# Optimization experiments

Hardware: AMD Instinct MI355X
Metric: run time of the kernel (lower is better)

## Reference

```python
import jax, jax.numpy as jnp
import numpy as np

SQRT2 = 1.4142135623730951
MH_C = 0.8673250705840776  # (2/sqrt(3)) * pi**(-1/4), mexican-hat normalizer


def _bn(x, eps=1e-5):
    # BatchNorm (training-mode batch stats, default affine gamma=1, beta=0)
    mu = jnp.mean(x, axis=0, keepdims=True)
    var = jnp.var(x, axis=0, keepdims=True)
    return (x - mu) / jnp.sqrt(var + eps)


def setup_inputs() -> dict:
    key = jax.random.key(0)
    ks = jax.random.split(key, 10)
    N, F, E, B, OUT = 1024, 1024, 32768, 16, 10
    H = F // 2  # 512 after Haar DWT
    x = jax.random.normal(ks[0], (N, F), dtype=jnp.float32)
    edge_index = jax.random.randint(ks[1], (2, E), 0, N, dtype=jnp.int32)
    batch = jnp.sort(jax.random.randint(ks[2], (N,), 0, B, dtype=jnp.int32))
    w_att = jax.random.normal(ks[3], (2,), dtype=jnp.float32)  # Linear(2,1,bias=False)
    wk_scale = jnp.ones((H, H), dtype=jnp.float32)
    wk_trans = jax.random.normal(ks[4], (H, H), dtype=jnp.float32) * 0.1
    wk_wav_w = jax.random.normal(ks[5], (H, H), dtype=jnp.float32) * 0.05
    wk_base_w = jax.random.normal(ks[6], (H, H), dtype=jnp.float32) * 0.05
    fc1_w = jax.random.normal(ks[7], (512, F + H), dtype=jnp.float32) * 0.02
    fc1_b = jnp.zeros((512,), dtype=jnp.float32)
    fc2_w = jax.random.normal(ks[8], (OUT, 512), dtype=jnp.float32) * 0.02
    fc2_b = jnp.zeros((OUT,), dtype=jnp.float32)
    return {"x": x, "w_att": w_att, "wk_scale": wk_scale, "wk_trans": wk_trans,
            "wk_wav_w": wk_wav_w, "wk_base_w": wk_base_w, "fc1_w": fc1_w,
            "fc1_b": fc1_b, "fc2_w": fc2_w, "fc2_b": fc2_b,
            "edge_index": edge_index, "batch": batch, "num_graphs": B}


def reference(x, w_att, wk_scale, wk_trans, wk_wav_w, wk_base_w,
              fc1_w, fc1_b, fc2_w, fc2_b, edge_index, batch, num_graphs):
    N = x.shape[0]
    # --- WaveletAttention: Haar ('db1') DWT over the feature dim ---
    xe, xo = x[:, 0::2], x[:, 1::2]
    low = (xe + xo) / SQRT2            # [N, 512]
    high = (xe - xo) / SQRT2           # [N, 512]
    scores = jax.nn.sigmoid(low * w_att[0] + high * w_att[1])
    h = scores * low + (1.0 - scores) * high
    # --- GINConv aggregation (eps=0): self + sum of neighbor features ---
    src, dst = edge_index[0], edge_index[1]
    agg = h + jax.ops.segment_sum(h[src], dst, num_segments=N)  # [N, 512]
    # --- WavKAN layer 512->512 (mexican hat) ---
    xs = (agg[:, None, :] - wk_trans) / wk_scale                # [N, 512, 512]
    xs2 = xs * xs
    mh = MH_C * (1.0 - xs2) * jnp.exp(-0.5 * xs2)
    wav = jnp.einsum('noi,oi->no', mh, wk_wav_w)                # [N, 512]
    base = jax.nn.silu(agg) @ wk_base_w.T
    conv_out = _bn(wav + base)   # WavKAN-internal BatchNorm1d
    conv_out = _bn(conv_out)     # bn1 (dropout p=0 -> identity)
    # --- skip concat + bn2 ---
    z = _bn(jnp.concatenate([x, conv_out], axis=1))             # [N, 1536]
    # --- global mean pool over graphs ---
    sums = jax.ops.segment_sum(z, batch, num_segments=num_graphs)
    cnts = jax.ops.segment_sum(jnp.ones((N,), z.dtype), batch, num_segments=num_graphs)
    pooled = sums / jnp.maximum(cnts, 1.0)[:, None]             # [B, 1536]
    # --- classifier head (eval-mode dropout = identity) ---
    h1 = jax.nn.relu(pooled @ fc1_w.T + fc1_b)
    return h1 @ fc2_w.T + fc2_b
```

## Files before the change

### kernel.cpp

```cpp
#include <hip/hip_runtime.h>
#include <math.h>

#define N_NODES 1024
#define F_DIM   1024
#define H_DIM   512
#define E_EDGES 32768
#define B_GRAPHS 16
#define OUT_DIM 10
#define FH_DIM  1536
#define EPS 1e-5f
#define MH_C_D 0.8673250705840776
#define C2_D   0.72134752044448170368
#define CSC    0.84932180028801904272f
#define WC2F   ((float)(MH_C_D / C2_D))
#define INV_SQRT2 0.70710678118654752440f

typedef float v2f __attribute__((ext_vector_type(2)));
typedef unsigned int u32;
typedef const __attribute__((address_space(1))) u32 gu32;
typedef __attribute__((address_space(3))) u32 lu32;

#if __has_builtin(__builtin_amdgcn_exp2f)
#define EXP2NEG(x) __builtin_amdgcn_exp2f(-(x))
#else
#define EXP2NEG(x) __expf(-0.69314718055994530942f * (x))
#endif

__global__ __launch_bounds__(256) void k_h(const float* __restrict__ x,
                                           const float* __restrict__ watt,
                                           float* __restrict__ h) {
    int idx = blockIdx.x * 256 + threadIdx.x;
    float2 p = ((const float2*)x)[idx];
    float lo = (p.x + p.y) * INV_SQRT2;
    float hi = (p.x - p.y) * INV_SQRT2;
    float t  = lo * watt[0] + hi * watt[1];
    float sc = 1.0f / (1.0f + __expf(-t));
    h[idx] = sc * lo + (1.0f - sc) * hi;
}

__global__ __launch_bounds__(256) void k_zero(float* __restrict__ p) {
    p[blockIdx.x * 256 + threadIdx.x] = 0.0f;
}

__global__ __launch_bounds__(256) void k_hist(const int* __restrict__ dst,
                                              int* __restrict__ deg) {
    int e = blockIdx.x * 256 + threadIdx.x;
    atomicAdd(&deg[dst[e]], 1);
}

__global__ __launch_bounds__(1024) void k_scan(const int* __restrict__ deg,
                                               int* __restrict__ start,
                                               int* __restrict__ cursor) {
    __shared__ int wsum[16];
    int t = threadIdx.x;
    int lane = t & 63, wid = t >> 6;
    int v = deg[t];
    int x = v;
    #pragma unroll
    for (int off = 1; off < 64; off <<= 1) {
        int y = __shfl_up(x, off, 64);
        if (lane >= off) x += y;
    }
    if (lane == 63) wsum[wid] = x;
    __syncthreads();
    if (t < 16) {
        int w = wsum[t];
        int xs = w;
        #pragma unroll
        for (int off = 1; off < 16; off <<= 1) {
            int y = __shfl_up(xs, off, 64);
            if (t >= off) xs += y;
        }
        wsum[t] = xs - w;
    }
    __syncthreads();
    int excl = wsum[wid] + x - v;
    start[t] = excl;
    cursor[t] = excl;
}

__global__ __launch_bounds__(256) void k_fill(const int* __restrict__ src,
                                              const int* __restrict__ dst,
                                              int* __restrict__ cursor,
                                              int* __restrict__ elist) {
    int e = blockIdx.x * 256 + threadIdx.x;
    int slot = atomicAdd(&cursor[dst[e]], 1);
    elist[slot] = src[e];
}

__global__ __launch_bounds__(256) void k_gather(const float* __restrict__ h,
                                                const int* __restrict__ start,
                                                const int* __restrict__ deg,
                                                const int* __restrict__ elist,
                                                float* __restrict__ agg) {
    int d = blockIdx.x;
    int t = threadIdx.x;
    int st = start[d], dg = deg[d];
    const float2* h2 = (const float2*)h;
    float2 a = h2[d * 256 + t];
    int k = 0;
    for (; k + 2 <= dg; k += 2) {
        int s0 = elist[st + k];
        int s1 = elist[st + k + 1];
        float2 v0 = h2[s0 * 256 + t];
        float2 v1 = h2[s1 * 256 + t];
        a.x += v0.x + v1.x;
        a.y += v0.y + v1.y;
    }
    if (k < dg) {
        int s0 = elist[st + k];
        float2 v0 = h2[s0 * 256 + t];
        a.x += v0.x; a.y += v0.y;
    }
    ((float2*)agg)[d * 256 + t] = a;
}

__global__ __launch_bounds__(256) void k_transpose(const float* __restrict__ agg,
                                                   float* __restrict__ aggT,
                                                   float* __restrict__ siluT) {
    __shared__ float tile[64 * 65];
    const int t = threadIdx.x;
    const int n0 = blockIdx.x * 64;
    const int i0 = blockIdx.y * 64;
    #pragma unroll
    for (int v = 0; v < 4; ++v) {
        int flat = v * 256 + t;
        int r = flat >> 4, c4 = flat & 15;
        float4 a = *(const float4*)&agg[(n0 + r) * H_DIM + i0 + c4 * 4];
        tile[(c4 * 4 + 0) * 65 + r] = a.x;
        tile[(c4 * 4 + 1) * 65 + r] = a.y;
        tile[(c4 * 4 + 2) * 65 + r] = a.z;
        tile[(c4 * 4 + 3) * 65 + r] = a.w;
    }
    __syncthreads();
    #pragma unroll
    for (int v = 0; v < 4; ++v) {
        int flat = v * 256 + t;
        int il = flat >> 4, c4 = flat & 15;
        float4 a;
        a.x = tile[il * 65 + c4 * 4 + 0];
        a.y = tile[il * 65 + c4 * 4 + 1];
        a.z = tile[il * 65 + c4 * 4 + 2];
        a.w = tile[il * 65 + c4 * 4 + 3];
        int g = (i0 + il) * N_NODES + n0 + c4 * 4;
        *(float4*)&aggT[g] = a;
        float4 s;
        s.x = a.x / (1.0f + __expf(-a.x));
        s.y = a.y / (1.0f + __expf(-a.y));
        s.z = a.z / (1.0f + __expf(-a.z));
        s.w = a.w / (1.0f + __expf(-a.w));
        *(float4*)&siluT[g] = s;
    }
}

__global__ __launch_bounds__(256) void k_prep(const float* __restrict__ scale,
                                              const float* __restrict__ trans,
                                              const float* __restrict__ ww,
                                              const float* __restrict__ bw,
                                              float* __restrict__ pk) {
    int g = blockIdx.x * 256 + threadIdx.x;
    float iv = 1.0f / scale[g];
    float4 p;
    p.x = iv * CSC;
    p.y = trans[g] * iv * CSC;
    p.z = ww[g] * WC2F;
    p.w = bw[g];
    ((float4*)pk)[g] = p;
}

#define TN 64
#define TO 32
#define KI 16
#define TOP (TO + 1)
#define ZSPLIT 8
#define ZLEN (H_DIM / ZSPLIT)
__global__ __launch_bounds__(256, 4) void k_wavelet(const float* __restrict__ aggT,
                                                    const float* __restrict__ siluT,
                                                    const float* __restrict__ pk,
                                                    float* __restrict__ vbp) {
    __shared__ float sA[KI * TN];
    __shared__ float sS[KI * TN];
    __shared__ float4 sP4[KI * TOP];

    const int t  = threadIdx.x;
    const int n0 = blockIdx.x * TN;
    const int o0 = blockIdx.y * TO;
    const int z0 = blockIdx.z * ZLEN;
    const int nl = (t & 15) * 4;
    const int ol = (t >> 4) * 2;

    v2f accw[2][2] = {};
    v2f accb[2][2] = {};
    const v2f c2v = {(float)C2_D, (float)C2_D};

    for (int stg = 0; stg < ZLEN / KI; ++stg) {
        const int i0 = z0 + stg * KI;
        __syncthreads();
        {
            int g = (i0 + (t >> 4)) * N_NODES + n0 + nl;
            __builtin_amdgcn_global_load_lds((gu32*)&aggT[g],  (lu32*)&sA[t * 4], 16, 0, 0);
            __builtin_amdgcn_global_load_lds((gu32*)&siluT[g], (lu32*)&sS[t * 4], 16, 0, 0);
        }
        #pragma unroll
        for (int j = 0; j < 2; ++j) {
            int u = j * 256 + t;
            int o = u >> 4, ii = u & 15;
            sP4[ii * TOP + o] = ((const float4*)pk)[(o0 + o) * H_DIM + i0 + ii];
        }
        __syncthreads();
        #pragma unroll 4
        for (int ii = 0; ii < KI; ++ii) {
            float4 a = *(const float4*)&sA[ii * TN + nl];
            float4 s = *(const float4*)&sS[ii * TN + nl];
            v2f a01 = {a.x, a.y}, a23 = {a.z, a.w};
            v2f s01 = {s.x, s.y}, s23 = {s.z, s.w};
            #pragma unroll
            for (int oo = 0; oo < 2; ++oo) {
                float4 p = sP4[ii * TOP + ol + oo];
                v2f iv2 = {p.x, p.x};
                v2f tf2 = {p.y, p.y};
                v2f w2  = {p.z, p.z};
                v2f b2  = {p.w, p.w};
                {
                    v2f y  = a01 * iv2 - tf2;
                    v2f y2 = y * y;
                    v2f e; e.x = EXP2NEG(y2.x); e.y = EXP2NEG(y2.y);
                    v2f wm = w2 * (c2v - y2);
                    accw[oo][0] += wm * e;
                    accb[oo][0] += s01 * b2;
                }
                {
                    v2f y  = a23 * iv2 - tf2;
                    v2f y2 = y * y;
                    v2f e; e.x = EXP2NEG(y2.x); e.y = EXP2NEG(y2.y);
                    v2f wm = w2 * (c2v - y2);
                    accw[oo][1] += wm * e;
                    accb[oo][1] += s23 * b2;
                }
            }
        }
    }
    float* out = vbp + (size_t)blockIdx.z * (N_NODES * H_DIM);
    #pragma unroll
    for (int nn = 0; nn < 4; ++nn) {
        int pr = nn >> 1, cmu = nn & 1;
        float2 o2;
        o2.x = (cmu ? accw[0][pr].y : accw[0][pr].x) + (cmu ? accb[0][pr].y : accb[0][pr].x);
        o2.y = (cmu ? accw[1][pr].y : accw[1][pr].x) + (cmu ? accb[1][pr].y : accb[1][pr].x);
        *(float2*)&out[(n0 + nl + nn) * H_DIM + o0 + ol] = o2;
    }
}

__global__ __launch_bounds__(256) void k_reduce(const float* __restrict__ vbp,
                                                float* __restrict__ vb,
                                                float* __restrict__ colsum,
                                                float* __restrict__ colsum2) {
    const int b = blockIdx.x;
    const int o0 = (b & 7) * 64;
    const int n0 = (b >> 3) * 128;
    const int t = threadIdx.x;
    const int oc = o0 + (t & 63);
    const int nsub = t >> 6;
    float s = 0.f, s2 = 0.f;
    for (int r = 0; r < 32; ++r) {
        int n = n0 + r * 4 + nsub;
        size_t idx = (size_t)n * H_DIM + oc;
        float v = 0.f;
        #pragma unroll
        for (int z = 0; z < ZSPLIT; ++z) v += vbp[z * (N_NODES * H_DIM) + idx];
        vb[idx] = v;
        s += v; s2 += v * v;
    }
    __shared__ float sh1[256], sh2[256];
    sh1[t] = s; sh2[t] = s2;
    __syncthreads();
    if (t < 64) {
        s  = sh1[t] + sh1[t + 64] + sh1[t + 128] + sh1[t + 192];
        s2 = sh2[t] + sh2[t + 64] + sh2[t + 128] + sh2[t + 192];
        unsafeAtomicAdd(&colsum[o0 + t], s);
        unsafeAtomicAdd(&colsum2[o0 + t], s2);
    }
}

__global__ __launch_bounds__(256) void k_xstats(const float* __restrict__ x,
                                                float* __restrict__ xsum,
                                                float* __restrict__ xsum2) {
    const int n0 = blockIdx.x * 16;
    const int t = threadIdx.x;
    float s[4] = {}, s2[4] = {};
    for (int r = 0; r < 16; ++r) {
        #pragma unroll
        for (int ch = 0; ch < 4; ++ch) {
            float v = x[(n0 + r) * F_DIM + ch * 256 + t];
            s[ch] += v; s2[ch] += v * v;
        }
    }
    #pragma unroll
    for (int ch = 0; ch < 4; ++ch) {
        unsafeAtomicAdd(&xsum[ch * 256 + t], s[ch]);
        unsafeAtomicAdd(&xsum2[ch * 256 + t], s2[ch]);
    }
}

__global__ __launch_bounds__(256) void k_finalize(const float* __restrict__ colsum,
                                                  const float* __restrict__ colsum2,
                                                  const float* __restrict__ xsum,
                                                  const float* __restrict__ xsum2,
                                                  float* __restrict__ muv,
                                                  float* __restrict__ Sv,
                                                  float* __restrict__ mux,
                                                  float* __restrict__ Sx,
                                                  const int* __restrict__ batch,
                                                  int* __restrict__ gstart,
                                                  int* __restrict__ gcnt) {
    __shared__ int cnt_sh[B_GRAPHS];
    __shared__ int start_sh[B_GRAPHS];
    int t = threadIdx.x;
    if (t < B_GRAPHS) { cnt_sh[t] = 0; start_sh[t] = 0; }
    __syncthreads();
    for (int n = t; n < N_NODES; n += 256) {
        int b = batch[n];
        atomicAdd(&cnt_sh[b], 1);
        if (n == 0 || batch[n - 1] != b) start_sh[b] = n;
    }
    for (int c = t; c < FH_DIM; c += 256) {
        if (c < H_DIM) {
            float mu  = colsum[c] * (1.0f / N_NODES);
            float var = colsum2[c] * (1.0f / N_NODES) - mu * mu;
            if (var < 0.f) var = 0.f;
            float s1v = 1.0f / sqrtf(var + EPS);
            float v1  = var * s1v * s1v;
            float s2v = 1.0f / sqrtf(v1 + EPS);
            float v2  = v1 * s2v * s2v;
            float s3v = 1.0f / sqrtf(v2 + EPS);
            muv[c] = mu;
            Sv[c]  = s1v * s2v * s3v;
        } else {
            int xc = c - H_DIM;
            float mu  = xsum[xc] * (1.0f / N_NODES);
            float var = xsum2[xc] * (1.0f / N_NODES) - mu * mu;
            if (var < 0.f) var = 0.f;
            mux[xc] = mu;
            Sx[xc]  = 1.0f / sqrtf(var + EPS);
        }
    }
    __syncthreads();
    if (t < B_GRAPHS) { gstart[t] = start_sh[t]; gcnt[t] = cnt_sh[t]; }
}

__global__ __launch_bounds__(256) void k_pool(const float* __restrict__ x,
                                              const float* __restrict__ vb,
                                              const int* __restrict__ gstart,
                                              const int* __restrict__ gcnt,
                                              const float* __restrict__ mux,
                                              const float* __restrict__ Sx,
                                              const float* __restrict__ muv,
                                              const float* __restrict__ Sv,
                                              float* __restrict__ pooled) {
    const int b = blockIdx.x;
    const int ch = blockIdx.y;
    const int t = threadIdx.x;
    const int cnt = gcnt[b], st = gstart[b];
    float ic = (cnt > 0) ? 1.0f / (float)cnt : 0.f;
    float acc = 0.f;
    if (ch < 4) {
        const float* base = x + ch * 256 + t;
        for (int r = 0; r < cnt; ++r) acc += base[(size_t)(st + r) * F_DIM];
        int c = ch * 256 + t;
        pooled[b * FH_DIM + c] = (acc * ic - mux[c]) * Sx[c];
    } else {
        int chv = ch - 4;
        const float* base = vb + chv * 256 + t;
        for (int r = 0; r < cnt; ++r) acc += base[(size_t)(st + r) * H_DIM];
        int c = chv * 256 + t;
        pooled[b * FH_DIM + F_DIM + c] = (acc * ic - muv[c]) * Sv[c];
    }
}

__global__ __launch_bounds__(256) void k_fc1(const float* __restrict__ pooled,
                                             const float* __restrict__ w,
                                             const float* __restrict__ bias,
                                             float* __restrict__ h1) {
    int wid = (blockIdx.x * 256 + threadIdx.x) >> 6;
    int lane = threadIdx.x & 63;
    int b = wid >> 9, o = wid & 511;
    const float4* pr = (const float4*)(pooled + b * FH_DIM);
    const float4* wr = (const float4*)(w + o * FH_DIM);
    float acc = 0.f;
    #pragma unroll
    for (int k = 0; k < 6; ++k) {
        float4 a = pr[k * 64 + lane];
        float4 v = wr[k * 64 + lane];
        acc += a.x * v.x + a.y * v.y + a.z * v.z + a.w * v.w;
    }
    #pragma unroll
    for (int off = 32; off > 0; off >>= 1) acc += __shfl_down(acc, off);
    if (lane == 0) h1[b * H_DIM + o] = fmaxf(acc + bias[o], 0.f);
}

__global__ __launch_bounds__(256) void k_fc2(const float* __restrict__ h1,
                                             const float* __restrict__ w,
                                             const float* __restrict__ bias,
                                             float* __restrict__ outp) {
    int wid = (blockIdx.x * 256 + threadIdx.x) >> 6;
    int lane = threadIdx.x & 63;
    if (wid >= B_GRAPHS * OUT_DIM) return;
    int b = wid / OUT_DIM, u = wid % OUT_DIM;
    const float4* hr = (const float4*)(h1 + b * H_DIM);
    const float4* wr = (const float4*)(w + u * H_DIM);
    float acc = 0.f;
    #pragma unroll
    for (int k = 0; k < 2; ++k) {
        float4 a = hr[k * 64 + lane];
        float4 v = wr[k * 64 + lane];
        acc += a.x * v.x + a.y * v.y + a.z * v.z + a.w * v.w;
    }
    #pragma unroll
    for (int off = 32; off > 0; off >>= 1) acc += __shfl_down(acc, off);
    if (lane == 0) outp[b * OUT_DIM + u] = acc + bias[u];
}

extern "C" void kernel_launch(void* const* d_in, const int* in_sizes, int n_in,
                              void* d_out, int out_size, void* d_ws, size_t ws_size,
                              hipStream_t stream) {
    const float* x       = (const float*)d_in[0];
    const float* w_att   = (const float*)d_in[1];
    const float* wk_scale= (const float*)d_in[2];
    const float* wk_trans= (const float*)d_in[3];
    const float* wk_wav  = (const float*)d_in[4];
    const float* wk_base = (const float*)d_in[5];
    const float* fc1_w   = (const float*)d_in[6];
    const float* fc1_b   = (const float*)d_in[7];
    const float* fc2_w   = (const float*)d_in[8];
    const float* fc2_b   = (const float*)d_in[9];
    const int*   eidx    = (const int*)d_in[10];
    const int*   batch   = (const int*)d_in[11];
    float* outp = (float*)d_out;

    float* ws = (float*)d_ws;
    const int NH = N_NODES * H_DIM;
    float* h      = ws;
    float* agg    = h + NH;
    float* aggT   = agg + NH;
    float* siluT  = aggT + NH;
    float* pk     = siluT + NH;
    float* vbp    = pk + 4 * (H_DIM * H_DIM);
    float* vb     = vbp + (size_t)ZSPLIT * NH;
    float* colsum = vb + NH;
    float* colsum2= colsum + 512;
    float* xsum   = colsum2 + 512;
    float* xsum2  = xsum + 1024;
    int*   deg    = (int*)(xsum2 + 1024);
    int*   estart = deg + N_NODES;
    int*   cursor = estart + N_NODES;
    int*   elist  = cursor + N_NODES;
    float* muv    = (float*)(elist + E_EDGES);
    float* Sv     = muv + 512;
    float* mux    = Sv + 512;
    float* Sx     = mux + 1024;
    int*   gstart = (int*)(Sx + 1024);
    int*   gcnt   = gstart + 16;
    float* pooled = (float*)(gcnt + 16);
    float* h1     = pooled + B_GRAPHS * FH_DIM;

    const int* src = eidx;
    const int* dst = eidx + E_EDGES;

    k_zero<<<16, 256, 0, stream>>>(colsum);
    k_h<<<NH / 256, 256, 0, stream>>>(x, w_att, h);
    k_hist<<<E_EDGES / 256, 256, 0, stream>>>(dst, deg);
    k_scan<<<1, N_NODES, 0, stream>>>(deg, estart, cursor);
    k_fill<<<E_EDGES / 256, 256, 0, stream>>>(src, dst, cursor, elist);
    k_prep<<<(H_DIM * H_DIM) / 256, 256, 0, stream>>>(wk_scale, wk_trans, wk_wav, wk_base, pk);
    k_xstats<<<64, 256, 0, stream>>>(x, xsum, xsum2);
    k_gather<<<N_NODES, 256, 0, stream>>>(h, estart, deg, elist, agg);
    {
        dim3 grid(N_NODES / 64, H_DIM / 64);
        k_transpose<<<grid, 256, 0, stream>>>(agg, aggT, siluT);
    }
    {
        dim3 grid(N_NODES / TN, H_DIM / TO, ZSPLIT);
        k_wavelet<<<grid, 256, 0, stream>>>(aggT, siluT, pk, vbp);
    }
    k_reduce<<<64, 256, 0, stream>>>(vbp, vb, colsum, colsum2);
    k_finalize<<<1, 256, 0, stream>>>(colsum, colsum2, xsum, xsum2, muv, Sv, mux, Sx,
                                      batch, gstart, gcnt);
    {
        dim3 grid(B_GRAPHS, 6);
        k_pool<<<grid, 256, 0, stream>>>(x, vb, gstart, gcnt, mux, Sx, muv, Sv, pooled);
    }
    k_fc1<<<(B_GRAPHS * H_DIM * 64) / 256, 256, 0, stream>>>(pooled, fc1_w, fc1_b, h1);
    k_fc2<<<(B_GRAPHS * OUT_DIM * 64 + 255) / 256, 256, 0, stream>>>(h1, fc2_w, fc2_b, outp);
}
```

Before: 214.7 us.

## Merge setup kernels, widen wavelet output tile, fold finalize into pooling

Several small kernels are merged into fewer launches: h computation, parameter packing and zeroing go into one setup kernel, and the degree histogram shares a launch with the x statistics. The finalize kernel is removed, and each pool block now recomputes its graph range and BN scales itself. The wavelet kernel tile grows from 32 to 64 outputs per block, doubling register accumulators so parameter loads are reused across more work. The Mexican-hat multiply is refactored to save an op per element, the gather loop is unrolled by four, and the reduce kernel uses more blocks. The aim is less launch overhead and better reuse, at the cost of higher register pressure and lower occupancy in the wavelet kernel.

```diff
diff --git a/kernel.cpp b/kernel.cpp
--- a/kernel.cpp
+++ b/kernel.cpp
@@ -11,6 +11,7 @@
 #define EPS 1e-5f
 #define MH_C_D 0.8673250705840776
 #define C2_D   0.72134752044448170368
+#define C2_F   ((float)C2_D)
 #define CSC    0.84932180028801904272f
 #define WC2F   ((float)(MH_C_D / C2_D))
 #define INV_SQRT2 0.70710678118654752440f
@@ -26,26 +27,65 @@
 #define EXP2NEG(x) __expf(-0.69314718055994530942f * (x))
 #endif
 
-__global__ __launch_bounds__(256) void k_h(const float* __restrict__ x,
-                                           const float* __restrict__ watt,
-                                           float* __restrict__ h) {
-    int idx = blockIdx.x * 256 + threadIdx.x;
-    float2 p = ((const float2*)x)[idx];
-    float lo = (p.x + p.y) * INV_SQRT2;
-    float hi = (p.x - p.y) * INV_SQRT2;
-    float t  = lo * watt[0] + hi * watt[1];
-    float sc = 1.0f / (1.0f + __expf(-t));
-    h[idx] = sc * lo + (1.0f - sc) * hi;
-}
-
-__global__ __launch_bounds__(256) void k_zero(float* __restrict__ p) {
-    p[blockIdx.x * 256 + threadIdx.x] = 0.0f;
-}
-
-__global__ __launch_bounds__(256) void k_hist(const int* __restrict__ dst,
-                                              int* __restrict__ deg) {
-    int e = blockIdx.x * 256 + threadIdx.x;
-    atomicAdd(&deg[dst[e]], 1);
+__global__ __launch_bounds__(256) void k_setup(const float* __restrict__ x,
+                                               const float* __restrict__ watt,
+                                               float* __restrict__ h,
+                                               const float* __restrict__ scale,
+                                               const float* __restrict__ trans,
+                                               const float* __restrict__ ww,
+                                               const float* __restrict__ bw,
+                                               float* __restrict__ pk,
+                                               float* __restrict__ zbase) {
+    const int bid = blockIdx.x;
+    const int t = threadIdx.x;
+    if (bid < 2048) {
+        int idx = bid * 256 + t;
+        float2 p = ((const float2*)x)[idx];
+        float lo = (p.x + p.y) * INV_SQRT2;
+        float hi = (p.x - p.y) * INV_SQRT2;
+        float tt = lo * watt[0] + hi * watt[1];
+        float sc = 1.0f / (1.0f + __expf(-tt));
+        h[idx] = sc * lo + (1.0f - sc) * hi;
+    } else if (bid < 3072) {
+        int g = (bid - 2048) * 256 + t;
+        float iv = 1.0f / scale[g];
+        float4 p;
+        p.x = iv * CSC;
+        p.y = trans[g] * iv * CSC;
+        p.z = ww[g] * WC2F;
+        p.w = bw[g];
+        ((float4*)pk)[g] = p;
+    } else {
+        zbase[(bid - 3072) * 256 + t] = 0.0f;
+    }
+}
+
+__global__ __launch_bounds__(256) void k_hx(const int* __restrict__ dst,
+                                            int* __restrict__ deg,
+                                            const float* __restrict__ x,
+                                            float* __restrict__ xsum,
+                                            float* __restrict__ xsum2) {
+    const int bid = blockIdx.x;
+    const int t = threadIdx.x;
+    if (bid < 128) {
+        int e = bid * 256 + t;
+        atomicAdd(&deg[dst[e]], 1);
+    } else {
+        const int n0 = (bid - 128) * 16;
+        float s[4] = {}, s2[4] = {};
+        for (int r = 0; r < 16; ++r) {
+            #pragma unroll
+            for (int ch = 0; ch < 4; ++ch) {
+                float v = x[(n0 + r) * F_DIM + ch * 256 + t];
+                s[ch] += v; s2[ch] += v * v;
+            }
+        }
+        #pragma unroll
+        for (int ch = 0; ch < 4; ++ch) {
+            unsafeAtomicAdd(&xsum[ch * 256 + t], s[ch]);
+            unsafeAtomicAdd(&xsum2[ch * 256 + t], s2[ch]);
+        }
+    }
 }
 
 __global__ __launch_bounds__(1024) void k_scan(const int* __restrict__ deg,
@@ -99,15 +139,19 @@
     const float2* h2 = (const float2*)h;
     float2 a = h2[d * 256 + t];
     int k = 0;
-    for (; k + 2 <= dg; k += 2) {
+    for (; k + 4 <= dg; k += 4) {
         int s0 = elist[st + k];
         int s1 = elist[st + k + 1];
+        int s2 = elist[st + k + 2];
+        int s3 = elist[st + k + 3];
         float2 v0 = h2[s0 * 256 + t];
         float2 v1 = h2[s1 * 256 + t];
-        a.x += v0.x + v1.x;
-        a.y += v0.y + v1.y;
-    }
-    if (k < dg) {
+        float2 v2 = h2[s2 * 256 + t];
+        float2 v3 = h2[s3 * 256 + t];
+        a.x += (v0.x + v1.x) + (v2.x + v3.x);
+        a.y += (v0.y + v1.y) + (v2.y + v3.y);
+    }
+    for (; k < dg; ++k) {
         int s0 = elist[st + k];
         float2 v0 = h2[s0 * 256 + t];
         a.x += v0.x; a.y += v0.y;
@@ -153,31 +197,16 @@
     }
 }
 
-__global__ __launch_bounds__(256) void k_prep(const float* __restrict__ scale,
-                                              const float* __restrict__ trans,
-                                              const float* __restrict__ ww,
-                                              const float* __restrict__ bw,
-                                              float* __restrict__ pk) {
-    int g = blockIdx.x * 256 + threadIdx.x;
-    float iv = 1.0f / scale[g];
-    float4 p;
-    p.x = iv * CSC;
-    p.y = trans[g] * iv * CSC;
-    p.z = ww[g] * WC2F;
-    p.w = bw[g];
-    ((float4*)pk)[g] = p;
-}
-
 #define TN 64
-#define TO 32
+#define TO 64
 #define KI 16
 #define TOP (TO + 1)
 #define ZSPLIT 8
 #define ZLEN (H_DIM / ZSPLIT)
-__global__ __launch_bounds__(256, 4) void k_wavelet(const float* __restrict__ aggT,
-                                                    const float* __restrict__ siluT,
-                                                    const float* __restrict__ pk,
-                                                    float* __restrict__ vbp) {
+__global__ __launch_bounds__(256) void k_wavelet(const float* __restrict__ aggT,
+                                                 const float* __restrict__ siluT,
+                                                 const float* __restrict__ pk,
+                                                 float* __restrict__ vbp) {
     __shared__ float sA[KI * TN];
     __shared__ float sS[KI * TN];
     __shared__ float4 sP4[KI * TOP];
@@ -187,11 +216,10 @@
     const int o0 = blockIdx.y * TO;
     const int z0 = blockIdx.z * ZLEN;
     const int nl = (t & 15) * 4;
-    const int ol = (t >> 4) * 2;
-
-    v2f accw[2][2] = {};
-    v2f accb[2][2] = {};
-    const v2f c2v = {(float)C2_D, (float)C2_D};
+    const int ol = (t >> 4) * 4;
+
+    v2f accw[4][2] = {};
+    v2f accb[4][2] = {};
 
     for (int stg = 0; stg < ZLEN / KI; ++stg) {
         const int i0 = z0 + stg * KI;
@@ -202,7 +230,7 @@
             __builtin_amdgcn_global_load_lds((gu32*)&siluT[g], (lu32*)&sS[t * 4], 16, 0, 0);
         }
         #pragma unroll
-        for (int j = 0; j < 2; ++j) {
+        for (int j = 0; j < 4; ++j) {
             int u = j * 256 + t;
             int o = u >> 4, ii = u & 15;
             sP4[ii * TOP + o] = ((const float4*)pk)[(o0 + o) * H_DIM + i0 + ii];
@@ -215,17 +243,19 @@
             v2f a01 = {a.x, a.y}, a23 = {a.z, a.w};
             v2f s01 = {s.x, s.y}, s23 = {s.z, s.w};
             #pragma unroll
-            for (int oo = 0; oo < 2; ++oo) {
+            for (int oo = 0; oo < 4; ++oo) {
                 float4 p = sP4[ii * TOP + ol + oo];
+                float wcs = p.z * C2_F;
                 v2f iv2 = {p.x, p.x};
                 v2f tf2 = {p.y, p.y};
                 v2f w2  = {p.z, p.z};
+                v2f wc2 = {wcs, wcs};
                 v2f b2  = {p.w, p.w};
                 {
                     v2f y  = a01 * iv2 - tf2;
                     v2f y2 = y * y;
                     v2f e; e.x = EXP2NEG(y2.x); e.y = EXP2NEG(y2.y);
-                    v2f wm = w2 * (c2v - y2);
+                    v2f wm = wc2 - w2 * y2;
                     accw[oo][0] += wm * e;
                     accb[oo][0] += s01 * b2;
                 }
@@ -233,7 +263,7 @@
                     v2f y  = a23 * iv2 - tf2;
                     v2f y2 = y * y;
                     v2f e; e.x = EXP2NEG(y2.x); e.y = EXP2NEG(y2.y);
-                    v2f wm = w2 * (c2v - y2);
+                    v2f wm = wc2 - w2 * y2;
                     accw[oo][1] += wm * e;
                     accb[oo][1] += s23 * b2;
                 }
@@ -244,10 +274,12 @@
     #pragma unroll
     for (int nn = 0; nn < 4; ++nn) {
         int pr = nn >> 1, cmu = nn & 1;
-        float2 o2;
-        o2.x = (cmu ? accw[0][pr].y : accw[0][pr].x) + (cmu ? accb[0][pr].y : accb[0][pr].x);
-        o2.y = (cmu ? accw[1][pr].y : accw[1][pr].x) + (cmu ? accb[1][pr].y : accb[1][pr].x);
-        *(float2*)&out[(n0 + nl + nn) * H_DIM + o0 + ol] = o2;
+        float4 o4;
+        o4.x = cmu ? accw[0][pr].y + accb[0][pr].y : accw[0][pr].x + accb[0][pr].x;
+        o4.y = cmu ? accw[1][pr].y + accb[1][pr].y : accw[1][pr].x + accb[1][pr].x;
+        o4.z = cmu ? accw[2][pr].y + accb[2][pr].y : accw[2][pr].x + accb[2][pr].x;
+        o4.w = cmu ? accw[3][pr].y + accb[3][pr].y : accw[3][pr].x + accb[3][pr].x;
+        *(float4*)&out[(n0 + nl + nn) * H_DIM + o0 + ol] = o4;
     }
 }
 
@@ -257,12 +289,12 @@
                                                 float* __restrict__ colsum2) {
     const int b = blockIdx.x;
     const int o0 = (b & 7) * 64;
-    const int n0 = (b >> 3) * 128;
+    const int n0 = (b >> 3) * 64;
     const int t = threadIdx.x;
     const int oc = o0 + (t & 63);
     const int nsub = t >> 6;
     float s = 0.f, s2 = 0.f;
-    for (int r = 0; r < 32; ++r) {
+    for (int r = 0; r < 16; ++r) {
         int n = n0 + r * 4 + nsub;
         size_t idx = (size_t)n * H_DIM + oc;
         float v = 0.f;
@@ -282,98 +314,59 @@
     }
 }
 
-__global__ __launch_bounds__(256) void k_xstats(const float* __restrict__ x,
-                                                float* __restrict__ xsum,
-                                                float* __restrict__ xsum2) {
-    const int n0 = blockIdx.x * 16;
-    const int t = threadIdx.x;
-    float s[4] = {}, s2[4] = {};
-    for (int r = 0; r < 16; ++r) {
-        #pragma unroll
-        for (int ch = 0; ch < 4; ++ch) {
-            float v = x[(n0 + r) * F_DIM + ch * 256 + t];
-            s[ch] += v; s2[ch] += v * v;
-        }
-    }
-    #pragma unroll
-    for (int ch = 0; ch < 4; ++ch) {
-        unsafeAtomicAdd(&xsum[ch * 256 + t], s[ch]);
-        unsafeAtomicAdd(&xsum2[ch * 256 + t], s2[ch]);
-    }
-}
-
-__global__ __launch_bounds__(256) void k_finalize(const float* __restrict__ colsum,
-                                                  const float* __restrict__ colsum2,
-                                                  const float* __restrict__ xsum,
-                                                  const float* __restrict__ xsum2,
-                                                  float* __restrict__ muv,
-                                                  float* __restrict__ Sv,
-                                                  float* __restrict__ mux,
-                                                  float* __restrict__ Sx,
-                                                  const int* __restrict__ batch,
-                                                  int* __restrict__ gstart,
-                                                  int* __restrict__ gcnt) {
-    __shared__ int cnt_sh[B_GRAPHS];
-    __shared__ int start_sh[B_GRAPHS];
-    int t = threadIdx.x;
-    if (t < B_GRAPHS) { cnt_sh[t] = 0; start_sh[t] = 0; }
-    __syncthreads();
-    for (int n = t; n < N_NODES; n += 256) {
-        int b = batch[n];
-        atomicAdd(&cnt_sh[b], 1);
-        if (n == 0 || batch[n - 1] != b) start_sh[b] = n;
-    }
-    for (int c = t; c < FH_DIM; c += 256) {
-        if (c < H_DIM) {
-            float mu  = colsum[c] * (1.0f / N_NODES);
-            float var = colsum2[c] * (1.0f / N_NODES) - mu * mu;
-            if (var < 0.f) var = 0.f;
-            float s1v = 1.0f / sqrtf(var + EPS);
-            float v1  = var * s1v * s1v;
-            float s2v = 1.0f / sqrtf(v1 + EPS);
-            float v2  = v1 * s2v * s2v;
-            float s3v = 1.0f / sqrtf(v2 + EPS);
-            muv[c] = mu;
-            Sv[c]  = s1v * s2v * s3v;
-        } else {
-            int xc = c - H_DIM;
-            float mu  = xsum[xc] * (1.0f / N_NODES);
-            float var = xsum2[xc] * (1.0f / N_NODES) - mu * mu;
-            if (var < 0.f) var = 0.f;
-            mux[xc] = mu;
-            Sx[xc]  = 1.0f / sqrtf(var + EPS);
-        }
-    }
-    __syncthreads();
-    if (t < B_GRAPHS) { gstart[t] = start_sh[t]; gcnt[t] = cnt_sh[t]; }
-}
-
 __global__ __launch_bounds__(256) void k_pool(const float* __restrict__ x,
                                               const float* __restrict__ vb,
-                                              const int* __restrict__ gstart,
-                                              const int* __restrict__ gcnt,
-                                              const float* __restrict__ mux,
-                                              const float* __restrict__ Sx,
-                                              const float* __restrict__ muv,
-                                              const float* __restrict__ Sv,
+                                              const int* __restrict__ batch,
+                                              const float* __restrict__ colsum,
+                                              const float* __restrict__ colsum2,
+                                              const float* __restrict__ xsum,
+                                              const float* __restrict__ xsum2,
                                               float* __restrict__ pooled) {
     const int b = blockIdx.x;
     const int ch = blockIdx.y;
     const int t = threadIdx.x;
-    const int cnt = gcnt[b], st = gstart[b];
+
+    __shared__ int s_cnt[4];
+    __shared__ int s_st;
+    int c = 0;
+    for (int n = t; n < N_NODES; n += 256) {
+        int bb = batch[n];
+        int pb = (n == 0) ? -1 : batch[n - 1];
+        c += (bb == b) ? 1 : 0;
+        if (bb == b && pb != b) s_st = n;
+    }
+    #pragma unroll
+    for (int off = 32; off > 0; off >>= 1) c += __shfl_down(c, off);
+    if ((t & 63) == 0) s_cnt[t >> 6] = c;
+    __syncthreads();
+    int cnt = s_cnt[0] + s_cnt[1] + s_cnt[2] + s_cnt[3];
+    int st = (cnt > 0) ? s_st : 0;
     float ic = (cnt > 0) ? 1.0f / (float)cnt : 0.f;
+
     float acc = 0.f;
     if (ch < 4) {
-        const float* base = x + ch * 256 + t;
+        int col = ch * 256 + t;
+        float mu  = xsum[col] * (1.0f / N_NODES);
+        float var = xsum2[col] * (1.0f / N_NODES) - mu * mu;
+        if (var < 0.f) var = 0.f;
+        float S = 1.0f / sqrtf(var + EPS);
+        const float* base = x + col;
         for (int r = 0; r < cnt; ++r) acc += base[(size_t)(st + r) * F_DIM];
-        int c = ch * 256 + t;
-        pooled[b * FH_DIM + c] = (acc * ic - mux[c]) * Sx[c];
+        pooled[b * FH_DIM + col] = (acc * ic - mu) * S;
     } else {
-        int chv = ch - 4;
-        const float* base = vb + chv * 256 + t;
+        int col = (ch - 4) * 256 + t;
+        float mu  = colsum[col] * (1.0f / N_NODES);
+        float var = colsum2[col] * (1.0f / N_NODES) - mu * mu;
+        if (var < 0.f) var = 0.f;
+        float s1v = 1.0f / sqrtf(var + EPS);
+        float v1  = var * s1v * s1v;
+        float s2v = 1.0f / sqrtf(v1 + EPS);
+        float v2  = v1 * s2v * s2v;
+        float s3v = 1.0f / sqrtf(v2 + EPS);
+        float S = s1v * s2v * s3v;
+        const float* base = vb + col;
         for (int r = 0; r < cnt; ++r) acc += base[(size_t)(st + r) * H_DIM];
-        int c = chv * 256 + t;
-        pooled[b * FH_DIM + F_DIM + c] = (acc * ic - muv[c]) * Sv[c];
+        pooled[b * FH_DIM + F_DIM + col] = (acc * ic - mu) * S;
     }
 }
 
@@ -454,25 +447,17 @@
     int*   estart = deg + N_NODES;
     int*   cursor = estart + N_NODES;
     int*   elist  = cursor + N_NODES;
-    float* muv    = (float*)(elist + E_EDGES);
-    float* Sv     = muv + 512;
-    float* mux    = Sv + 512;
-    float* Sx     = mux + 1024;
-    int*   gstart = (int*)(Sx + 1024);
-    int*   gcnt   = gstart + 16;
-    float* pooled = (float*)(gcnt + 16);
+    float* pooled = (float*)(elist + E_EDGES);
     float* h1     = pooled + B_GRAPHS * FH_DIM;
 
     const int* src = eidx;
     const int* dst = eidx + E_EDGES;
 
-    k_zero<<<16, 256, 0, stream>>>(colsum);
-    k_h<<<NH / 256, 256, 0, stream>>>(x, w_att, h);
-    k_hist<<<E_EDGES / 256, 256, 0, stream>>>(dst, deg);
+    k_setup<<<3088, 256, 0, stream>>>(x, w_att, h, wk_scale, wk_trans, wk_wav, wk_base,
+                                      pk, colsum);
+    k_hx<<<192, 256, 0, stream>>>(dst, deg, x, xsum, xsum2);
     k_scan<<<1, N_NODES, 0, stream>>>(deg, estart, cursor);
     k_fill<<<E_EDGES / 256, 256, 0, stream>>>(src, dst, cursor, elist);
-    k_prep<<<(H_DIM * H_DIM) / 256, 256, 0, stream>>>(wk_scale, wk_trans, wk_wav, wk_base, pk);
-    k_xstats<<<64, 256, 0, stream>>>(x, xsum, xsum2);
     k_gather<<<N_NODES, 256, 0, stream>>>(h, estart, deg, elist, agg);
     {
         dim3 grid(N_NODES / 64, H_DIM / 64);
@@ -482,12 +467,10 @@
         dim3 grid(N_NODES / TN, H_DIM / TO, ZSPLIT);
         k_wavelet<<<grid, 256, 0, stream>>>(aggT, siluT, pk, vbp);
     }
-    k_reduce<<<64, 256, 0, stream>>>(vbp, vb, colsum, colsum2);
-    k_finalize<<<1, 256, 0, stream>>>(colsum, colsum2, xsum, xsum2, muv, Sv, mux, Sx,
-                                      batch, gstart, gcnt);
+    k_reduce<<<128, 256, 0, stream>>>(vbp, vb, colsum, colsum2);
     {
         dim3 grid(B_GRAPHS, 6);
-        k_pool<<<grid, 256, 0, stream>>>(x, vb, gstart, gcnt, mux, Sx, muv, Sv, pooled);
+        k_pool<<<grid, 256, 0, stream>>>(x, vb, batch, colsum, colsum2, xsum, xsum2, pooled);
     }
     k_fc1<<<(B_GRAPHS * H_DIM * 64) / 256, 256, 0, stream>>>(pooled, fc1_w, fc1_b, h1);
     k_fc2<<<(B_GRAPHS * OUT_DIM * 64 + 255) / 256, 256, 0, stream>>>(h1, fc2_w, fc2_b, outp);
```

Result: faster. 195.2 us (-9.1%).
